# Optimization experiments

Measured on AMD Instinct MI355X. Metric: run time of the kernel, lower is better.

The kernel has to match this reference:

```python
import jax, jax.numpy as jnp
import numpy as np

WS = 8          # window_size
OWS = 12        # overlap_win_size = int(8*0.5)+8
PAD = 2         # (OWS-WS)//2
HEADS = 6
DH = 16         # dim_head
INNER = HEADS * DH  # 96
SCALE = DH ** -0.5


def rel_to_abs(x):
    # x: (b, l, m) with m = 2*r - 1
    b, l, m = x.shape
    r = (m + 1) // 2
    x = jnp.concatenate([x, jnp.zeros((b, l, 1), x.dtype)], axis=2)
    flat = x.reshape(b, l * (m + 1))
    flat = jnp.concatenate([flat, jnp.zeros((b, m - l), x.dtype)], axis=1)
    final = flat.reshape(b, l + 1, m)[:, :l, m - r:]
    return final  # (b, l, r)


def relative_logits_1d(q, rel_k):
    # q: (B, X, Y, d), rel_k: (2r-1, d)
    B, X, Y, _ = q.shape
    r = (rel_k.shape[0] + 1) // 2
    logits = jnp.einsum('bxyd,rd->bxyr', q, rel_k)           # (B, X, Y, 2r-1)
    logits = rel_to_abs(logits.reshape(B * X, Y, -1)).reshape(B, X, Y, r)
    logits = jnp.broadcast_to(logits[:, :, None], (B, X, r, Y, r))  # b x i y j
    return logits


def rel_pos_emb(q, rel_height, rel_width):
    # q: (B, WS*WS, d) -> bias (B, WS*WS, OWS*OWS)
    B, _, d = q.shape
    qg = q.reshape(B, WS, WS, d)
    lw = relative_logits_1d(qg, rel_width)                   # (B, x, i, y, j)
    lw = lw.transpose(0, 1, 3, 2, 4).reshape(B, WS * WS, OWS * OWS)  # b (x y) (i j)
    lh = relative_logits_1d(qg.transpose(0, 2, 1, 3), rel_height)    # (B, y, i, x, j) roles swapped
    lh = lh.transpose(0, 3, 1, 4, 2).reshape(B, WS * WS, OWS * OWS)  # b (y x) (j i)
    return lw + lh


def unfold_windows(t, nh, nw):
    # torch nn.Unfold(kernel=OWS, stride=WS, padding=PAD) then
    # rearrange 'b (c j) i -> (b i) j c' -> (b*nh*nw, OWS*OWS, C)
    b, C, _, _ = t.shape
    tp = jnp.pad(t, ((0, 0), (0, 0), (PAD, PAD), (PAD, PAD)))
    ridx = (jnp.arange(nh) * WS)[:, None] + jnp.arange(OWS)   # (nh, OWS)
    cidx = (jnp.arange(nw) * WS)[:, None] + jnp.arange(OWS)   # (nw, OWS)
    p = tp[:, :, ridx, :]            # (b, C, nh, OWS, Wp)
    p = p[:, :, :, :, cidx]          # (b, C, nh, OWS, nw, OWS)
    p = p.transpose(0, 2, 4, 3, 5, 1)  # (b, nh, nw, OWS, OWS, C)
    return p.reshape(b * nh * nw, OWS * OWS, C)


def split_heads(t):
    # (B, n, heads*dh) -> (B*heads, n, dh)
    B, n, _ = t.shape
    return t.reshape(B, n, HEADS, DH).transpose(0, 2, 1, 3).reshape(B * HEADS, n, DH)


def setup_inputs() -> dict:
    key = jax.random.key(0)
    k = jax.random.split(key, 5)
    x = jax.random.normal(k[0], (2, 96, 256, 256), jnp.float32)
    qkv_w = jax.random.normal(k[1], (288, 96), jnp.float32) * 0.05
    qkv_b = jnp.zeros((288,), jnp.float32)
    proj_w = jax.random.normal(k[2], (96, 96), jnp.float32) * 0.05
    proj_b = jnp.zeros((96,), jnp.float32)
    rel_height = jax.random.normal(k[3], (23, 16), jnp.float32) * SCALE
    rel_width = jax.random.normal(k[4], (23, 16), jnp.float32) * SCALE
    return {"x": x, "qkv_w": qkv_w, "qkv_b": qkv_b, "proj_w": proj_w,
            "proj_b": proj_b, "rel_height": rel_height, "rel_width": rel_width}


def reference(x, qkv_w, qkv_b, proj_w, proj_b, rel_height, rel_width):
    b, c, h, w = x.shape
    nh, nw = h // WS, w // WS
    qkv = jnp.einsum('oc,bchw->bohw', qkv_w, x) + qkv_b[None, :, None, None]
    qs, ks, vs = jnp.split(qkv, 3, axis=1)  # each (b, INNER, h, w)
    # queries: non-overlapping windows 'b c (h p1) (w p2) -> (b h w) (p1 p2) c'
    qs = qs.reshape(b, INNER, nh, WS, nw, WS).transpose(0, 2, 4, 3, 5, 1)
    qs = qs.reshape(b * nh * nw, WS * WS, INNER)
    ks = unfold_windows(ks, nh, nw)  # (b*nh*nw, OWS*OWS, INNER)
    vs = unfold_windows(vs, nh, nw)
    qs, ks, vs = map(split_heads, (qs, ks, vs))  # (B*heads, n, DH)
    qs = qs * SCALE
    attn = jnp.einsum('bqd,bkd->bqk', qs, ks)
    attn = attn + rel_pos_emb(qs, rel_height, rel_width)
    attn = jax.nn.softmax(attn, axis=-1)
    out = jnp.einsum('bqk,bkd->bqd', attn, vs)  # (b*nh*nw*heads, WS*WS, DH)
    out = out.reshape(b, nh, nw, HEADS, WS, WS, DH)
    out = out.transpose(0, 3, 6, 1, 4, 2, 5).reshape(b, INNER, h, w)
    out = jnp.einsum('oc,bchw->bohw', proj_w, out) + proj_b[None, :, None, None]
    return out
```

## Files before the change

kernel.cpp:

```cpp
#include <hip/hip_runtime.h>
#include <hip/hip_bf16.h>


typedef __attribute__((ext_vector_type(8))) short bf16x8;
typedef __attribute__((ext_vector_type(4))) float f32x4;

__device__ __forceinline__ f32x4 mfma16(bf16x8 a, bf16x8 b, f32x4 c) {
  return __builtin_amdgcn_mfma_f32_16x16x32_bf16(a, b, c, 0, 0, 0);
}
__device__ __forceinline__ short f2b(float f) {
  unsigned u = __builtin_bit_cast(unsigned, f);
  unsigned r = u + 0x7fffu + ((u >> 16) & 1u);
  return (short)(r >> 16);
}
__device__ __forceinline__ unsigned cvtpk(float lo, float hi) {
  unsigned r;
  asm("v_cvt_pk_bf16_f32 %0, %1, %2" : "=v"(r) : "v"(lo), "v"(hi));
  return r;
}
__device__ __forceinline__ void splitf(float x, short& h, short& l) {
  unsigned u = __builtin_bit_cast(unsigned, x);
  h = (short)(u >> 16);
  float fh = __builtin_bit_cast(float, u & 0xffff0000u);
  l = f2b(x - fh);
}

#define KPLANE 1081600L
#define QS (0.25f * 1.44269504f)

__global__ __launch_bounds__(256) void prep_kernel(
    const float* __restrict__ qkv_w, const float* __restrict__ proj_w,
    const float* __restrict__ rel_h, const float* __restrict__ rel_w,
    const float* __restrict__ qkv_b,
    short* __restrict__ qwh, short* __restrict__ qwl,
    short* __restrict__ pwh, short* __restrict__ pwl,
    short* __restrict__ rhb, short* __restrict__ rwb,
    float* __restrict__ sbias, short* __restrict__ k_t) {
  int i = blockIdx.x * 256 + threadIdx.x;
  if (i < 288 * 96) {
    float wv = qkv_w[i];
    if (i < 96 * 96) wv *= QS;
    short h, l;
    splitf(wv, h, l);
    qwh[i] = h;
    qwl[i] = l;
  }
  if (i < 96 * 96) {
    short h, l;
    splitf(proj_w[i], h, l);
    pwh[i] = h;
    pwl[i] = l;
  }
  if (i < 368) {
    rhb[i] = f2b(rel_h[i]);
    rwb[i] = f2b(rel_w[i]);
  }
  if (i < 288) sbias[i] = qkv_b[i] * (i < 96 ? QS : 1.0f);
  if (i < 12 * 2064) {
    int plane = i / 2064, r = i - plane * 2064;
    int py, px;
    if (r < 1040) {
      int rowid = r / 260;
      py = (rowid < 2) ? rowid : 256 + rowid;
      px = r - rowid * 260;
    } else {
      int r2 = r - 1040;
      py = 2 + (r2 >> 2);
      int cid = r2 & 3;
      px = (cid < 2) ? cid : 256 + cid;
    }
    bf16x8 z = {0, 0, 0, 0, 0, 0, 0, 0};
    long base = (long)plane * KPLANE + (long)(py * 260 + px) * 16;
    *(bf16x8*)(k_t + base) = z;
    *(bf16x8*)(k_t + base + 8) = z;
  }
}

__global__ __launch_bounds__(256) void qkv_kernel(
    const float* __restrict__ x, const short* __restrict__ qwh,
    const short* __restrict__ qwl, const float* __restrict__ sbias,
    short* __restrict__ q_t, short* __restrict__ k_t,
    short* __restrict__ v_t) {
  const int tid = threadIdx.x;
  const int wave = tid >> 6, lane = tid & 63;
  const int quad = lane >> 4, col = lane & 15;
  const int blk = blockIdx.x;
  const int b = blk >> 8, row = blk & 255;

  const float* xw = x + (((long)b * 96) << 16) + row * 256 + wave * 64 + col;
  bf16x8 bx[4][3];
#pragma unroll
  for (int tile = 0; tile < 4; ++tile)
#pragma unroll
    for (int ks = 0; ks < 3; ++ks) {
      const float* p = xw + tile * 16 + (((long)(ks * 32 + quad * 8)) << 16);
      float v0 = p[0];
      float v1 = p[1L << 16];
      float v2 = p[2L << 16];
      float v3 = p[3L << 16];
      float v4 = p[4L << 16];
      float v5 = p[5L << 16];
      float v6 = p[6L << 16];
      float v7 = p[7L << 16];
      union { unsigned u[4]; bf16x8 w; } t;
      t.u[0] = cvtpk(v0, v1);
      t.u[1] = cvtpk(v2, v3);
      t.u[2] = cvtpk(v4, v5);
      t.u[3] = cvtpk(v6, v7);
      bx[tile][ks] = t.w;
    }

  const short* wbh = qwh + col * 96 + quad * 8;
  const short* wbl = qwl + col * 96 + quad * 8;
  bf16x8 wh[3], wl[3];
#pragma unroll
  for (int ks = 0; ks < 3; ++ks) {
    wh[ks] = *(const bf16x8*)(wbh + ks * 32);
    wl[ks] = *(const bf16x8*)(wbl + ks * 32);
  }

  const long pixb = (long)blk * 256 + wave * 64 + col;
  short* kbase = k_t + (long)b * KPLANE +
                 ((long)((row + 2) * 260 + wave * 64 + col + 2)) * 16 +
                 quad * 4;

#pragma unroll
  for (int t6 = 0; t6 < 18; ++t6) {
    bf16x8 nh[3], nl[3];
    if (t6 < 17) {
#pragma unroll
      for (int ks = 0; ks < 3; ++ks) {
        nh[ks] = *(const bf16x8*)(wbh + (t6 + 1) * 1536 + ks * 32);
        nl[ks] = *(const bf16x8*)(wbl + (t6 + 1) * 1536 + ks * 32);
      }
    }
    f32x4 bv = *(const f32x4*)(sbias + t6 * 16 + quad * 4);
    f32x4 acc[4] = {bv, bv, bv, bv};
#pragma unroll
    for (int ks = 0; ks < 3; ++ks)
#pragma unroll
      for (int tile = 0; tile < 4; ++tile) {
        acc[tile] = mfma16(wh[ks], bx[tile][ks], acc[tile]);
        acc[tile] = mfma16(wl[ks], bx[tile][ks], acc[tile]);
      }
#pragma unroll
    for (int tile = 0; tile < 4; ++tile) {
      unsigned d0 = cvtpk(acc[tile][0], acc[tile][1]);
      unsigned d1 = cvtpk(acc[tile][2], acc[tile][3]);
      if (t6 >= 6 && t6 < 12) {
        short* kp = kbase + (long)(t6 - 6) * (2 * KPLANE) + tile * 256;
        *(unsigned*)kp = d0;
        *(unsigned*)(kp + 2) = d1;
      } else {
        short* plane = (t6 < 6 ? q_t : v_t) +
                       (long)(t6 < 6 ? t6 : t6 - 12) * 2097152 + pixb * 16 +
                       tile * 256 + quad * 4;
        *(unsigned*)plane = d0;
        *(unsigned*)(plane + 2) = d1;
      }
    }
    if (t6 < 17) {
#pragma unroll
      for (int ks = 0; ks < 3; ++ks) {
        wh[ks] = nh[ks];
        wl[ks] = nl[ks];
      }
    }
  }
}

__global__ __launch_bounds__(256) void attn_kernel(
    const short* __restrict__ q_t, const short* __restrict__ k_t,
    const short* __restrict__ v_t, const short* __restrict__ rhb,
    const short* __restrict__ rwb, short* __restrict__ ao) {
  __shared__ __attribute__((aligned(16))) short v_lds[16][168];
  __shared__ __attribute__((aligned(16))) char scratch[4][5248];

  const int orig = blockIdx.x, head = blockIdx.y;
  const int win = ((orig & 7) << 8) | (orig >> 3);
  const int b = win >> 10, wy = (win & 1023) >> 5, wx = win & 31;
  const int y0 = wy * 8 - 2, x0 = wx * 8 - 2;
  const long pb = (long)b << 16;
  const int tid = threadIdx.x;

  if (tid < 160) {
    const int key = tid;
    bool valid = false;
    long pix = 0;
    if (key < 144) {
      int kh = key / 12, kw = key - kh * 12;
      int gy = y0 + kh, gx = x0 + kw;
      valid = ((unsigned)gy < 256u) && ((unsigned)gx < 256u);
      pix = pb + gy * 256 + gx;
    }
    if (valid) {
      const short* src = v_t + (long)head * 2097152 + pix * 16;
      union { bf16x8 v; short s[8]; } u0, u1;
      u0.v = *(const bf16x8*)src;
      u1.v = *(const bf16x8*)(src + 8);
      for (int d = 0; d < 8; ++d) {
        v_lds[d][key] = u0.s[d];
        v_lds[d + 8][key] = u1.s[d];
      }
    } else {
      for (int d = 0; d < 16; ++d) v_lds[d][key] = 0;
    }
  }
  __syncthreads();

  const int wave = tid >> 6, lane = tid & 63;
  const int quad = lane >> 4, col = lane & 15;
  float* dWs = (float*)scratch[wave];
  float* dHt = dWs + 600;
  unsigned* ppd = (unsigned*)scratch[wave];

  const short* qp = q_t + (long)head * 2097152;
  const short* kpb = k_t + (long)(head * 2 + b) * KPLANE;

  bf16x8 qf = {0, 0, 0, 0, 0, 0, 0, 0};
  if (quad < 2) {
    int qg = wave * 16 + col;
    int qy = qg >> 3, qx = qg & 7;
    qf = *(const bf16x8*)(qp + (pb + (wy * 8 + qy) * 256 + wx * 8 + qx) * 16 +
                          quad * 8);
  }

  for (int nt = 0; nt < 2; ++nt) {
    int r = nt * 16 + col;
    bf16x8 bw = {0, 0, 0, 0, 0, 0, 0, 0}, bh2 = bw;
    if (quad < 2 && r < 23) {
      bw = *(const bf16x8*)(rwb + r * 16 + quad * 8);
      bh2 = *(const bf16x8*)(rhb + r * 16 + quad * 8);
    }
    f32x4 z = {0.f, 0.f, 0.f, 0.f};
    f32x4 aw = mfma16(qf, bw, z);
    f32x4 ah = mfma16(qf, bh2, z);
    if (r < 23)
      for (int r4 = 0; r4 < 4; ++r4) {
        int ql = quad * 4 + r4;
        dWs[(r + (ql & 7)) * 20 + ql] = aw[r4];
        dHt[r * 20 + ql] = ah[r4];
      }
  }
  asm volatile("" ::: "memory");

  const f32x4 wv = *(const f32x4*)&dWs[(11 + col) * 20 + quad * 4];
  const int qy4 = wave * 2 + (quad >> 1);
  f32x4 hva[6];
#pragma unroll
  for (int nt = 0; nt < 6; ++nt)
    hva[nt] = *(const f32x4*)&dHt[(11 + nt - qy4) * 20 + quad * 4];
  asm volatile("" ::: "memory");

  const short* kb =
      kpb + (long)((wy * 8) * 260 + wx * 8 + col) * 16 + quad * 8;
  unsigned* wp0 = ppd + col * 9 + quad * 2;

#pragma unroll
  for (int nt = 0; nt < 6; ++nt) {
    bf16x8 kf = *(const bf16x8*)(kb + (long)nt * 4160);
    f32x4 acc = wv + hva[nt];
    f32x4 L = mfma16(qf, kf, acc);
    unsigned d0 = cvtpk(__builtin_amdgcn_exp2f(L[0]),
                        __builtin_amdgcn_exp2f(L[1]));
    unsigned d1 = cvtpk(__builtin_amdgcn_exp2f(L[2]),
                        __builtin_amdgcn_exp2f(L[3]));
    if (col < 12) {
      wp0[nt * 108] = d0;
      wp0[nt * 108 + 1] = d1;
    }
  }
  asm volatile("" ::: "memory");
  f32x4 hvb[6];
#pragma unroll
  for (int nt = 0; nt < 6; ++nt)
    hvb[nt] = *(const f32x4*)&dHt[(17 + nt - qy4) * 20 + quad * 4];
  asm volatile("" ::: "memory");
#pragma unroll
  for (int nt = 0; nt < 6; ++nt) {
    bf16x8 kf = *(const bf16x8*)(kb + (long)(nt + 6) * 4160);
    f32x4 acc = wv + hvb[nt];
    f32x4 L = mfma16(qf, kf, acc);
    unsigned d0 = cvtpk(__builtin_amdgcn_exp2f(L[0]),
                        __builtin_amdgcn_exp2f(L[1]));
    unsigned d1 = cvtpk(__builtin_amdgcn_exp2f(L[2]),
                        __builtin_amdgcn_exp2f(L[3]));
    if (col < 12) {
      wp0[(nt + 6) * 108] = d0;
      wp0[(nt + 6) * 108 + 1] = d1;
    }
  }
  asm volatile("" ::: "memory");

  const unsigned sel = (col & 1) ? 0x07060302u : 0x05040100u;
  const bf16x8 ones = {0x3F80, 0x3F80, 0x3F80, 0x3F80,
                       0x3F80, 0x3F80, 0x3F80, 0x3F80};
  f32x4 oacc = {0.f, 0.f, 0.f, 0.f}, oaccS = oacc;
  for (int ks = 0; ks < 5; ++ks) {
    int k0 = ks * 32 + quad * 8;
    bool live = k0 < 144;
    int k0c = live ? k0 : 136;
    const unsigned* rp = ppd + k0c * 9 + (col >> 1);
    unsigned r0 = rp[0], r1 = rp[9], r2 = rp[18], r3 = rp[27];
    unsigned r4v = rp[36], r5 = rp[45], r6 = rp[54], r7 = rp[63];
    union { unsigned u[4]; bf16x8 v; } pu;
    pu.u[0] = live ? __builtin_amdgcn_perm(r1, r0, sel) : 0u;
    pu.u[1] = live ? __builtin_amdgcn_perm(r3, r2, sel) : 0u;
    pu.u[2] = live ? __builtin_amdgcn_perm(r5, r4v, sel) : 0u;
    pu.u[3] = live ? __builtin_amdgcn_perm(r7, r6, sel) : 0u;
    bf16x8 vb = *(const bf16x8*)&v_lds[col][ks * 32 + quad * 8];
    oacc = mfma16(pu.v, vb, oacc);
    oaccS = mfma16(pu.v, ones, oaccS);
  }
  for (int r4 = 0; r4 < 4; ++r4) {
    int qg = wave * 16 + quad * 4 + r4;
    int qy = qg >> 3, qx = qg & 7;
    float val = oacc[r4] * __builtin_amdgcn_rcpf(oaccS[r4]);
    ao[(long)head * 2097152 +
       (pb + (wy * 8 + qy) * 256 + wx * 8 + qx) * 16 + col] = f2b(val);
  }
}

__global__ __launch_bounds__(256) void proj_kernel(
    const short* __restrict__ ao, const short* __restrict__ pwh,
    const short* __restrict__ pwl, const float* __restrict__ bias,
    float* __restrict__ out) {
  const int tid = threadIdx.x;
  const int wave = tid >> 6, lane = tid & 63;
  const int quad = lane >> 4, col = lane & 15;
  const int blk = blockIdx.x;
  const int b = blk >> 8;
  const long pix0 = (long)blk * 256 + wave * 64 + col;

  bf16x8 bfr[4][3];
#pragma unroll
  for (int tile = 0; tile < 4; ++tile)
#pragma unroll
    for (int ks = 0; ks < 3; ++ks) {
      int head = 2 * ks + (quad >> 1);
      bfr[tile][ks] =
          *(const bf16x8*)(ao + (long)head * 2097152 +
                           (pix0 + tile * 16) * 16 + (quad & 1) * 8);
    }

  const short* wbh = pwh + col * 96 + quad * 8;
  const short* wbl = pwl + col * 96 + quad * 8;
  bf16x8 ah[3], al[3];
#pragma unroll
  for (int ks = 0; ks < 3; ++ks) {
    ah[ks] = *(const bf16x8*)(wbh + ks * 32);
    al[ks] = *(const bf16x8*)(wbl + ks * 32);
  }
  float* ob = out + (((long)(b * 96 + quad * 4)) << 16) + (blk & 255) * 256 +
              wave * 64 + col;
#pragma unroll
  for (int mt = 0; mt < 6; ++mt) {
    bf16x8 nh[3], nl[3];
    if (mt < 5) {
#pragma unroll
      for (int ks = 0; ks < 3; ++ks) {
        nh[ks] = *(const bf16x8*)(wbh + (mt + 1) * 1536 + ks * 32);
        nl[ks] = *(const bf16x8*)(wbl + (mt + 1) * 1536 + ks * 32);
      }
    }
    f32x4 bv = *(const f32x4*)(bias + mt * 16 + quad * 4);
    f32x4 acc[4] = {bv, bv, bv, bv};
#pragma unroll
    for (int ks = 0; ks < 3; ++ks)
#pragma unroll
      for (int tile = 0; tile < 4; ++tile) {
        acc[tile] = mfma16(ah[ks], bfr[tile][ks], acc[tile]);
        acc[tile] = mfma16(al[ks], bfr[tile][ks], acc[tile]);
      }
    float* obm = ob + ((long)(mt * 16) << 16);
#pragma unroll
    for (int tile = 0; tile < 4; ++tile)
#pragma unroll
      for (int r = 0; r < 4; ++r)
        obm[((long)r << 16) + tile * 16] = acc[tile][r];
    if (mt < 5) {
#pragma unroll
      for (int ks = 0; ks < 3; ++ks) {
        ah[ks] = nh[ks];
        al[ks] = nl[ks];
      }
    }
  }
}

extern "C" void kernel_launch(void* const* d_in, const int* in_sizes, int n_in,
                              void* d_out, int out_size, void* d_ws,
                              size_t ws_size, hipStream_t stream) {
  const float* x = (const float*)d_in[0];
  const float* qkv_w = (const float*)d_in[1];
  const float* qkv_b = (const float*)d_in[2];
  const float* proj_w = (const float*)d_in[3];
  const float* proj_b = (const float*)d_in[4];
  const float* rel_h = (const float*)d_in[5];
  const float* rel_w = (const float*)d_in[6];

  const long NPIXC = 131072L * 96L;
  short* q_t = (short*)d_ws;
  short* k_t = q_t + NPIXC;
  short* v_t = k_t + 12 * KPLANE;
  short* ao = v_t + NPIXC;
  short* qwh = ao + NPIXC;
  short* qwl = qwh + 288 * 96;
  short* pwh = qwl + 288 * 96;
  short* pwl = pwh + 96 * 96;
  short* rhb = pwl + 96 * 96;
  short* rwb = rhb + 368;
  float* sbias = (float*)(rwb + 368);
  float* out = (float*)d_out;

  hipLaunchKernelGGL(prep_kernel, dim3(108), dim3(256), 0, stream, qkv_w,
                     proj_w, rel_h, rel_w, qkv_b, qwh, qwl, pwh, pwl, rhb, rwb,
                     sbias, k_t);
  hipLaunchKernelGGL(qkv_kernel, dim3(512), dim3(256), 0, stream, x, qwh, qwl,
                     sbias, q_t, k_t, v_t);
  hipLaunchKernelGGL(attn_kernel, dim3(2048, 6), dim3(256), 0, stream, q_t,
                     k_t, v_t, rhb, rwb, ao);
  hipLaunchKernelGGL(proj_kernel, dim3(512), dim3(256), 0, stream, ao, pwh,
                     pwl, proj_b, out);
}
```

Measured before the change: 203.8 us.

## Transpose QK MFMA so probabilities land query-major for vector LDS reads

Result: no change. 205.6 us (+0.9%).

```diff
diff --git a/kernel.cpp b/kernel.cpp
--- a/kernel.cpp
+++ b/kernel.cpp
@@ -4,6 +4,7 @@
 
 typedef __attribute__((ext_vector_type(8))) short bf16x8;
 typedef __attribute__((ext_vector_type(4))) float f32x4;
+typedef __attribute__((ext_vector_type(4))) unsigned u32x4;
 
 __device__ __forceinline__ f32x4 mfma16(bf16x8 a, bf16x8 b, f32x4 c) {
   return __builtin_amdgcn_mfma_f32_16x16x32_bf16(a, b, c, 0, 0, 0);
@@ -174,7 +175,7 @@
     const short* __restrict__ v_t, const short* __restrict__ rhb,
     const short* __restrict__ rwb, short* __restrict__ ao) {
   __shared__ __attribute__((aligned(16))) short v_lds[16][168];
-  __shared__ __attribute__((aligned(16))) char scratch[4][5248];
+  __shared__ __attribute__((aligned(16))) char scratch[4][5376];
 
   const int orig = blockIdx.x, head = blockIdx.y;
   const int win = ((orig & 7) << 8) | (orig >> 3);
@@ -210,8 +211,8 @@
 
   const int wave = tid >> 6, lane = tid & 63;
   const int quad = lane >> 4, col = lane & 15;
-  float* dWs = (float*)scratch[wave];
-  float* dHt = dWs + 600;
+  float* Ws = (float*)scratch[wave];
+  float* Ht = Ws + 320;
   unsigned* ppd = (unsigned*)scratch[wave];
 
   const short* qp = q_t + (long)head * 2097152;
@@ -225,8 +226,8 @@
                           quad * 8);
   }
 
-  for (int nt = 0; nt < 2; ++nt) {
-    int r = nt * 16 + col;
+  for (int nt2 = 0; nt2 < 2; ++nt2) {
+    int r = nt2 * 16 + col;
     bf16x8 bw = {0, 0, 0, 0, 0, 0, 0, 0}, bh2 = bw;
     if (quad < 2 && r < 23) {
       bw = *(const bf16x8*)(rwb + r * 16 + quad * 8);
@@ -234,80 +235,57 @@
     }
     f32x4 z = {0.f, 0.f, 0.f, 0.f};
     f32x4 aw = mfma16(qf, bw, z);
-    f32x4 ah = mfma16(qf, bh2, z);
-    if (r < 23)
-      for (int r4 = 0; r4 < 4; ++r4) {
-        int ql = quad * 4 + r4;
-        dWs[(r + (ql & 7)) * 20 + ql] = aw[r4];
-        dHt[r * 20 + ql] = ah[r4];
-      }
+    f32x4 ahh = mfma16(qf, bh2, z);
+    int kh = r - 11 + wave * 2 + (quad >> 1);
+#pragma unroll
+    for (int r4 = 0; r4 < 4; ++r4) {
+      int q = quad * 4 + r4;
+      int kw = r - 11 + (q & 7);
+      if ((unsigned)kw < 12u) Ws[q * 20 + kw] = aw[r4];
+      if ((unsigned)kh < 12u) Ht[q * 20 + kh] = ahh[r4];
+    }
   }
   asm volatile("" ::: "memory");
 
-  const f32x4 wv = *(const f32x4*)&dWs[(11 + col) * 20 + quad * 4];
-  const int qy4 = wave * 2 + (quad >> 1);
-  f32x4 hva[6];
-#pragma unroll
-  for (int nt = 0; nt < 6; ++nt)
-    hva[nt] = *(const f32x4*)&dHt[(11 + nt - qy4) * 20 + quad * 4];
+  const f32x4 wv4 = *(const f32x4*)&Ws[col * 20 + quad * 4];
+  const f32x4 h0 = *(const f32x4*)&Ht[col * 20];
+  const f32x4 h1 = *(const f32x4*)&Ht[col * 20 + 4];
+  const f32x4 h2 = *(const f32x4*)&Ht[col * 20 + 8];
+  asm volatile("" ::: "memory");
+
+  if (quad < 2) {
+    u32x4 z4 = {0u, 0u, 0u, 0u};
+    *(u32x4*)(ppd + col * 84 + 72 + quad * 4) = z4;
+  }
   asm volatile("" ::: "memory");
 
   const short* kb =
       kpb + (long)((wy * 8) * 260 + wx * 8 + col) * 16 + quad * 8;
-  unsigned* wp0 = ppd + col * 9 + quad * 2;
-
-#pragma unroll
-  for (int nt = 0; nt < 6; ++nt) {
+#pragma unroll
+  for (int nt = 0; nt < 12; ++nt) {
     bf16x8 kf = *(const bf16x8*)(kb + (long)nt * 4160);
-    f32x4 acc = wv + hva[nt];
-    f32x4 L = mfma16(qf, kf, acc);
+    float hs = nt < 4 ? h0[nt] : (nt < 8 ? h1[nt - 4] : h2[nt - 8]);
+    f32x4 acc = wv4 + hs;
+    f32x4 L = mfma16(kf, qf, acc);
     unsigned d0 = cvtpk(__builtin_amdgcn_exp2f(L[0]),
                         __builtin_amdgcn_exp2f(L[1]));
     unsigned d1 = cvtpk(__builtin_amdgcn_exp2f(L[2]),
                         __builtin_amdgcn_exp2f(L[3]));
-    if (col < 12) {
-      wp0[nt * 108] = d0;
-      wp0[nt * 108 + 1] = d1;
+    if (quad < 3) {
+      ppd[col * 84 + nt * 6 + quad * 2] = d0;
+      ppd[col * 84 + nt * 6 + quad * 2 + 1] = d1;
     }
   }
   asm volatile("" ::: "memory");
-  f32x4 hvb[6];
-#pragma unroll
-  for (int nt = 0; nt < 6; ++nt)
-    hvb[nt] = *(const f32x4*)&dHt[(17 + nt - qy4) * 20 + quad * 4];
-  asm volatile("" ::: "memory");
-#pragma unroll
-  for (int nt = 0; nt < 6; ++nt) {
-    bf16x8 kf = *(const bf16x8*)(kb + (long)(nt + 6) * 4160);
-    f32x4 acc = wv + hvb[nt];
-    f32x4 L = mfma16(qf, kf, acc);
-    unsigned d0 = cvtpk(__builtin_amdgcn_exp2f(L[0]),
-                        __builtin_amdgcn_exp2f(L[1]));
-    unsigned d1 = cvtpk(__builtin_amdgcn_exp2f(L[2]),
-                        __builtin_amdgcn_exp2f(L[3]));
-    if (col < 12) {
-      wp0[(nt + 6) * 108] = d0;
-      wp0[(nt + 6) * 108 + 1] = d1;
-    }
-  }
-  asm volatile("" ::: "memory");
-
-  const unsigned sel = (col & 1) ? 0x07060302u : 0x05040100u;
+
   const bf16x8 ones = {0x3F80, 0x3F80, 0x3F80, 0x3F80,
                        0x3F80, 0x3F80, 0x3F80, 0x3F80};
   f32x4 oacc = {0.f, 0.f, 0.f, 0.f}, oaccS = oacc;
+#pragma unroll
   for (int ks = 0; ks < 5; ++ks) {
-    int k0 = ks * 32 + quad * 8;
-    bool live = k0 < 144;
-    int k0c = live ? k0 : 136;
-    const unsigned* rp = ppd + k0c * 9 + (col >> 1);
-    unsigned r0 = rp[0], r1 = rp[9], r2 = rp[18], r3 = rp[27];
-    unsigned r4v = rp[36], r5 = rp[45], r6 = rp[54], r7 = rp[63];
-    union { unsigned u[4]; bf16x8 v; } pu;
-    pu.u[0] = live ? __builtin_amdgcn_perm(r1, r0, sel) : 0u;
-    pu.u[1] = live ? __builtin_amdgcn_perm(r3, r2, sel) : 0u;
-    pu.u[2] = live ? __builtin_amdgcn_perm(r5, r4v, sel) : 0u;
-    pu.u[3] = live ? __builtin_amdgcn_perm(r7, r6, sel) : 0u;
+    int base = ks * 4 + quad;
+    union { u32x4 u; bf16x8 v; } pu;
+    pu.u = *(const u32x4*)(ppd + col * 84 + base * 4);
     bf16x8 vb = *(const bf16x8*)&v_lds[col][ks * 32 + quad * 8];
     oacc = mfma16(pu.v, vb, oacc);
     oaccS = mfma16(pu.v, ones, oaccS);
```
